# Kernel optimization log

Measured on AMD Instinct MI355X. Metric: run time of the kernel, lower is better.

The kernel has to match this reference:

```python
import jax, jax.numpy as jnp
import numpy as np

N = 50000; E = 800000; B = 5000
ND = 32; ED = 16; HD = 64; H = 128; L = 3
IN_DIM = ND + 2 * H  # 288, GNN in_channels
NEG = 0.2  # GATv2 leaky_relu slope
EPS = 1e-5  # LayerNorm eps


def silu(x):
    return x * jax.nn.sigmoid(x)


def layer_norm(x, g, b):
    mu = jnp.mean(x, -1, keepdims=True)
    v = jnp.var(x, -1, keepdims=True)
    return (x - mu) * jax.lax.rsqrt(v + EPS) * g + b


def setup_inputs() -> dict:
    key = jax.random.key(0)
    ks = iter(jax.random.split(key, 48))

    def w(shape):
        return jax.random.normal(next(ks), shape, jnp.float32) * 0.02

    inp = {}
    inp['x_t'] = jax.random.normal(next(ks), (N, ND), jnp.float32)
    inp['t'] = jax.random.randint(next(ks), (N,), 0, 1000)
    inp['household_features'] = jax.random.normal(next(ks), (B, HD), jnp.float32)
    inp['edge_index'] = jax.random.randint(next(ks), (2, E), 0, N)
    inp['edge_attr'] = jax.random.normal(next(ks), (E, ED), jnp.float32)
    inp['batch'] = jnp.sort(jax.random.randint(next(ks), (N,), 0, B))
    z = jnp.zeros; o = jnp.ones
    inp.update(dict(
        tW1=w((1, H)), tb1=z(H), tW2=w((H, H)), tb2=z(H),
        hW1=w((HD, H)), hb1=z(H), hg1=o(H), hB1=z(H),
        hW2=w((H, H)), hb2=z(H), hg2=o(H), hB2=z(H),
        Wl=w((L, IN_DIM, H)), bl=z((L, H)), Wr=w((L, IN_DIM, H)), br=z((L, H)),
        We=w((L, ED, H)), att=w((L, H)), gb=z((L, H)),
        fcpW=w((H, IN_DIM)), fcpb=z(IN_DIM),
        npW1=w((H, H)), npb1=z(H), npg=o(H), npB=z(H),
        npW2=w((H, ND)), npb2=z(ND)))
    return inp


def reference(x_t, t, household_features, edge_index, edge_attr, batch,
              tW1, tb1, tW2, tb2,
              hW1, hb1, hg1, hB1, hW2, hb2, hg2, hB2,
              Wl, bl, Wr, br, We, att, gb,
              fcpW, fcpb, npW1, npb1, npg, npB, npW2, npb2):
    # time embedding: Linear(1,H) -> SiLU -> Linear(H,H)
    t_emb = silu(t[:, None].astype(jnp.float32) @ tW1 + tb1) @ tW2 + tb2
    # household encoder: (Linear, LN, SiLU) x2, then gather per node
    h = silu(layer_norm(household_features @ hW1 + hb1, hg1, hB1))
    h = silu(layer_norm(h @ hW2 + hb2, hg2, hB2))
    x = jnp.concatenate([x_t, t_emb, h[batch]], axis=1)  # [N, IN_DIM]

    # add self loops (PyG default), edge_attr filled with per-feature mean
    loop = jnp.arange(N)
    src = jnp.concatenate([edge_index[0], loop])
    dst = jnp.concatenate([edge_index[1], loop])
    ea = jnp.concatenate([edge_attr, jnp.broadcast_to(edge_attr.mean(0), (N, ED))], axis=0)

    for l in range(L):  # GATv2Conv layers (heads=1)
        xl = x @ Wl[l] + bl[l]  # [N, H] source transform
        xr = x @ Wr[l] + br[l]  # [N, H] target transform
        m = jax.nn.leaky_relu(xl[src] + xr[dst] + ea @ We[l], NEG)  # [Etot, H]
        score = m @ att[l]  # [Etot]
        smax = jax.ops.segment_max(score, dst, num_segments=N)
        ex = jnp.exp(score - smax[dst])
        denom = jax.ops.segment_sum(ex, dst, num_segments=N) + 1e-16
        alpha = ex / denom[dst]
        out = jax.ops.segment_sum(alpha[:, None] * xl[src], dst, num_segments=N) + gb[l]
        x = silu(out)
        if l < L - 1:
            x = x @ fcpW + fcpb  # fc_projection back to IN_DIM
    # node_projection: Linear, LN, SiLU, Linear
    return silu(layer_norm(x @ npW1 + npb1, npg, npB)) @ npW2 + npb2
```

## Files before the change

### kernel.cpp

```cpp
#include <hip/hip_runtime.h>
#include <hip/hip_bf16.h>

#define NN 50000
#define NE 800000
#define NB 5000
#define ND 32
#define EDD 16
#define HDD 64
#define H 128
#define ETOT (NE + NN)
#define NEG 0.2f
#define EPS_LN 1e-5f

typedef float pf2 __attribute__((ext_vector_type(2)));

__device__ __forceinline__ float siluf(float x){ return x / (1.f + __expf(-x)); }

__device__ __forceinline__ float wsum(float v){
  v += __shfl_xor(v, 32, 64);
  v += __shfl_xor(v, 16, 64);
  v += __shfl_xor(v, 8, 64);
  v += __shfl_xor(v, 4, 64);
  v += __shfl_xor(v, 2, 64);
  v += __shfl_xor(v, 1, 64);
  return v;
}

#define DPP_ADD(v, ctrl) \
  v += __builtin_bit_cast(float, __builtin_amdgcn_update_dpp(0, __builtin_bit_cast(int, v), ctrl, 0xf, 0xf, true))
__device__ __forceinline__ float wsum_bcast(float v){
  DPP_ADD(v, 0x111);
  DPP_ADD(v, 0x112);
  DPP_ADD(v, 0x114);
  DPP_ADD(v, 0x118);
  DPP_ADD(v, 0x142);
  DPP_ADD(v, 0x143);
  return __builtin_bit_cast(float, __builtin_amdgcn_readlane(__builtin_bit_cast(int, v), 63));
}

__device__ __forceinline__ float blockLN128(float x, const float* g, const float* b, int j, float* red){
  int lane = j & 63, wid = j >> 6;
  float s = wsum(x);
  if (lane == 0) red[wid] = s;
  __syncthreads();
  float mu = (red[0] + red[1]) * 0.0078125f;
  float d = x - mu;
  float s2 = wsum(d * d);
  if (lane == 0) red[2 + wid] = s2;
  __syncthreads();
  float var = (red[2] + red[3]) * 0.0078125f;
  return d * (1.f / sqrtf(var + EPS_LN)) * g[j] + b[j];
}

__global__ __launch_bounds__(128) void k_house(const float* __restrict__ hf,
    const float* __restrict__ hW1, const float* __restrict__ hb1,
    const float* __restrict__ hg1, const float* __restrict__ hB1,
    const float* __restrict__ hW2, const float* __restrict__ hb2,
    const float* __restrict__ hg2, const float* __restrict__ hB2,
    float* __restrict__ hout){
  __shared__ float sin_[HDD];
  __shared__ float smid[H];
  __shared__ float red[4];
  int bidx = blockIdx.x, j = threadIdx.x;
  if (j < HDD) sin_[j] = hf[bidx * HDD + j];
  __syncthreads();
  float acc = hb1[j];
  #pragma unroll
  for (int k = 0; k < HDD; k++) acc += sin_[k] * hW1[k * H + j];
  float v = siluf(blockLN128(acc, hg1, hB1, j, red));
  __syncthreads();
  smid[j] = v;
  __syncthreads();
  float acc2 = hb2[j];
  #pragma unroll
  for (int k = 0; k < H; k++) acc2 += smid[k] * hW2[k * H + j];
  float v2 = siluf(blockLN128(acc2, hg2, hB2, j, red));
  hout[bidx * H + j] = v2;
}

__global__ __launch_bounds__(128) void k_temb(const float* __restrict__ tW1, const float* __restrict__ tb1,
    const float* __restrict__ tW2, const float* __restrict__ tb2, float* __restrict__ table){
  __shared__ float smid[H];
  int bidx = blockIdx.x, j = threadIdx.x;
  float tv = (float)bidx;
  smid[j] = siluf(tv * tW1[j] + tb1[j]);
  __syncthreads();
  float acc = tb2[j];
  #pragma unroll
  for (int k = 0; k < H; k++) acc += smid[k] * tW2[k * H + j];
  table[bidx * H + j] = acc;
}

__global__ __launch_bounds__(256) void k_gemm(const float* __restrict__ A, const float* __restrict__ W,
    const float* __restrict__ bias, float* __restrict__ C, int M, int K, int Nc){
  __shared__ float As[16][68];
  __shared__ float Ws[16][64];
  int t = threadIdx.x;
  int m0 = blockIdx.x * 64, n0 = blockIdx.y * 64;
  int tx = t & 15, ty = t >> 4;
  int la_m = t >> 2, la_k = (t & 3) << 2;
  int lw_k = t >> 4, lw_j = (t & 15) << 2;
  float acc[4][4] = {{0.f}};
  int arow = m0 + la_m;
  for (int k0 = 0; k0 < K; k0 += 16){
    float4 a = make_float4(0.f, 0.f, 0.f, 0.f);
    if (arow < M) a = *(const float4*)(A + (size_t)arow * K + k0 + la_k);
    As[la_k + 0][la_m] = a.x; As[la_k + 1][la_m] = a.y;
    As[la_k + 2][la_m] = a.z; As[la_k + 3][la_m] = a.w;
    float4 wv = make_float4(0.f, 0.f, 0.f, 0.f);
    if (n0 + lw_j < Nc) wv = *(const float4*)(W + (size_t)(k0 + lw_k) * Nc + n0 + lw_j);
    *(float4*)&Ws[lw_k][lw_j] = wv;
    __syncthreads();
    #pragma unroll
    for (int k = 0; k < 16; k++){
      float4 a4 = *(const float4*)&As[k][ty << 2];
      float4 b4 = *(const float4*)&Ws[k][tx << 2];
      acc[0][0] += a4.x * b4.x; acc[0][1] += a4.x * b4.y; acc[0][2] += a4.x * b4.z; acc[0][3] += a4.x * b4.w;
      acc[1][0] += a4.y * b4.x; acc[1][1] += a4.y * b4.y; acc[1][2] += a4.y * b4.z; acc[1][3] += a4.y * b4.w;
      acc[2][0] += a4.z * b4.x; acc[2][1] += a4.z * b4.y; acc[2][2] += a4.z * b4.z; acc[2][3] += a4.z * b4.w;
      acc[3][0] += a4.w * b4.x; acc[3][1] += a4.w * b4.y; acc[3][2] += a4.w * b4.z; acc[3][3] += a4.w * b4.w;
    }
    __syncthreads();
  }
  int col = n0 + (tx << 2);
  if (col < Nc){
    float4 b4 = make_float4(0.f, 0.f, 0.f, 0.f);
    if (bias) b4 = *(const float4*)(bias + col);
    #pragma unroll
    for (int r = 0; r < 4; r++){
      int row = m0 + (ty << 2) + r;
      if (row < M){
        float4 o = make_float4(acc[r][0] + b4.x, acc[r][1] + b4.y, acc[r][2] + b4.z, acc[r][3] + b4.w);
        *(float4*)(C + (size_t)row * Nc + col) = o;
      }
    }
  }
}

__global__ __launch_bounds__(256) void k_gemm128(const float* __restrict__ A, const float* __restrict__ W,
    const float* __restrict__ bias, float* __restrict__ C, int M, int K, int Nc){
  __shared__ float As[16][132];
  __shared__ float Ws[16][128];
  int t = threadIdx.x;
  int m0 = blockIdx.x * 128, n0 = blockIdx.y * 128;
  int tx = t & 15, ty = t >> 4;
  float acc[8][8];
  #pragma unroll
  for (int r = 0; r < 8; r++)
    #pragma unroll
    for (int c = 0; c < 8; c++) acc[r][c] = 0.f;
  for (int k0 = 0; k0 < K; k0 += 16){
    #pragma unroll
    for (int l = 0; l < 2; l++){
      int idx = t + l * 256;
      int ar = idx >> 2, ac = (idx & 3) << 2;
      float4 a = make_float4(0.f, 0.f, 0.f, 0.f);
      if (m0 + ar < M) a = *(const float4*)(A + (size_t)(m0 + ar) * K + k0 + ac);
      As[ac + 0][ar] = a.x; As[ac + 1][ar] = a.y;
      As[ac + 2][ar] = a.z; As[ac + 3][ar] = a.w;
    }
    #pragma unroll
    for (int l = 0; l < 2; l++){
      int idx = t + l * 256;
      int wr = idx >> 5, wc = (idx & 31) << 2;
      float4 wv = make_float4(0.f, 0.f, 0.f, 0.f);
      if (n0 + wc < Nc) wv = *(const float4*)(W + (size_t)(k0 + wr) * Nc + n0 + wc);
      *(float4*)&Ws[wr][wc] = wv;
    }
    __syncthreads();
    #pragma unroll
    for (int k = 0; k < 16; k++){
      float4 a0 = *(const float4*)&As[k][ty * 8];
      float4 a1 = *(const float4*)&As[k][ty * 8 + 4];
      float4 b0 = *(const float4*)&Ws[k][tx * 8];
      float4 b1 = *(const float4*)&Ws[k][tx * 8 + 4];
      float ar_[8] = {a0.x, a0.y, a0.z, a0.w, a1.x, a1.y, a1.z, a1.w};
      float bc_[8] = {b0.x, b0.y, b0.z, b0.w, b1.x, b1.y, b1.z, b1.w};
      #pragma unroll
      for (int r = 0; r < 8; r++)
        #pragma unroll
        for (int c = 0; c < 8; c++) acc[r][c] += ar_[r] * bc_[c];
    }
    __syncthreads();
  }
  int col = n0 + tx * 8;
  float4 bb0 = make_float4(0.f, 0.f, 0.f, 0.f), bb1 = bb0;
  if (bias && col < Nc){ bb0 = *(const float4*)(bias + col); bb1 = *(const float4*)(bias + col + 4); }
  #pragma unroll
  for (int r = 0; r < 8; r++){
    int row = m0 + ty * 8 + r;
    if (row < M && col < Nc){
      float4 o0 = make_float4(acc[r][0] + bb0.x, acc[r][1] + bb0.y, acc[r][2] + bb0.z, acc[r][3] + bb0.w);
      float4 o1 = make_float4(acc[r][4] + bb1.x, acc[r][5] + bb1.y, acc[r][6] + bb1.z, acc[r][7] + bb1.w);
      *(float4*)(C + (size_t)row * Nc + col) = o0;
      *(float4*)(C + (size_t)row * Nc + col + 4) = o1;
    }
  }
}

__global__ __launch_bounds__(256) void k_gemmln(const float* __restrict__ A, const float* __restrict__ W,
    const float* __restrict__ bias, const float* __restrict__ g, const float* __restrict__ B,
    float* __restrict__ out, int M){
  __shared__ float As[16][132];
  __shared__ float Ws[16][128];
  int t = threadIdx.x;
  int m0 = blockIdx.x * 128;
  int tx = t & 15, ty = t >> 4;
  float acc[8][8];
  #pragma unroll
  for (int r = 0; r < 8; r++)
    #pragma unroll
    for (int c = 0; c < 8; c++) acc[r][c] = 0.f;
  for (int k0 = 0; k0 < H; k0 += 16){
    #pragma unroll
    for (int l = 0; l < 2; l++){
      int idx = t + l * 256;
      int ar = idx >> 2, ac = (idx & 3) << 2;
      float4 a = make_float4(0.f, 0.f, 0.f, 0.f);
      if (m0 + ar < M) a = *(const float4*)(A + (size_t)(m0 + ar) * H + k0 + ac);
      As[ac + 0][ar] = a.x; As[ac + 1][ar] = a.y;
      As[ac + 2][ar] = a.z; As[ac + 3][ar] = a.w;
    }
    #pragma unroll
    for (int l = 0; l < 2; l++){
      int idx = t + l * 256;
      int wr = idx >> 5, wc = (idx & 31) << 2;
      *(float4*)&Ws[wr][wc] = *(const float4*)(W + (size_t)(k0 + wr) * H + wc);
    }
    __syncthreads();
    #pragma unroll
    for (int k = 0; k < 16; k++){
      float4 a0 = *(const float4*)&As[k][ty * 8];
      float4 a1 = *(const float4*)&As[k][ty * 8 + 4];
      float4 b0 = *(const float4*)&Ws[k][tx * 8];
      float4 b1 = *(const float4*)&Ws[k][tx * 8 + 4];
      float ar_[8] = {a0.x, a0.y, a0.z, a0.w, a1.x, a1.y, a1.z, a1.w};
      float bc_[8] = {b0.x, b0.y, b0.z, b0.w, b1.x, b1.y, b1.z, b1.w};
      #pragma unroll
      for (int r = 0; r < 8; r++)
        #pragma unroll
        for (int c = 0; c < 8; c++) acc[r][c] += ar_[r] * bc_[c];
    }
    __syncthreads();
  }
  int col = tx * 8;
  float bb[8], gv[8], Bv[8];
  *(float4*)&bb[0] = *(const float4*)(bias + col); *(float4*)&bb[4] = *(const float4*)(bias + col + 4);
  *(float4*)&gv[0] = *(const float4*)(g + col);    *(float4*)&gv[4] = *(const float4*)(g + col + 4);
  *(float4*)&Bv[0] = *(const float4*)(B + col);    *(float4*)&Bv[4] = *(const float4*)(B + col + 4);
  #pragma unroll
  for (int r = 0; r < 8; r++){
    int row = m0 + ty * 8 + r;
    if (row >= M) continue;
    float v[8];
    float s = 0.f;
    #pragma unroll
    for (int c = 0; c < 8; c++){ v[c] = acc[r][c] + bb[c]; s += v[c]; }
    s += __shfl_xor(s, 1, 16); s += __shfl_xor(s, 2, 16);
    s += __shfl_xor(s, 4, 16); s += __shfl_xor(s, 8, 16);
    float mu = s * 0.0078125f;
    float s2 = 0.f;
    #pragma unroll
    for (int c = 0; c < 8; c++){ v[c] -= mu; s2 += v[c] * v[c]; }
    s2 += __shfl_xor(s2, 1, 16); s2 += __shfl_xor(s2, 2, 16);
    s2 += __shfl_xor(s2, 4, 16); s2 += __shfl_xor(s2, 8, 16);
    float rstd = 1.f / sqrtf(s2 * 0.0078125f + EPS_LN);
    float o[8];
    #pragma unroll
    for (int c = 0; c < 8; c++) o[c] = siluf(v[c] * rstd * gv[c] + Bv[c]);
    *(float4*)(out + (size_t)row * H + col) = *(float4*)&o[0];
    *(float4*)(out + (size_t)row * H + col + 4) = *(float4*)&o[4];
  }
}

__global__ void k_packs(const float* __restrict__ Wl, const float* __restrict__ Wr,
    float* __restrict__ W0h, float* __restrict__ W0m, float* __restrict__ W0t,
    float* __restrict__ Wp1, float* __restrict__ Wp2){
  int r = blockIdx.x, L = blockIdx.y, c = threadIdx.x;
  float v = (c < H) ? Wl[(size_t)L * 288 * H + r * H + c] : Wr[(size_t)L * 288 * H + r * H + (c - H)];
  if (L == 0){
    if (r < 32) W0h[r * 256 + c] = v;
    else if (r < 160) W0m[(r - 32) * 256 + c] = v;
    else W0t[(r - 160) * 256 + c] = v;
  } else {
    (L == 1 ? Wp1 : Wp2)[r * 256 + c] = v;
  }
}
__global__ void k_small(const float* __restrict__ bl, const float* __restrict__ br,
    const float* __restrict__ Wl, const float* __restrict__ Wr, const float* __restrict__ fcpb,
    float* __restrict__ b0, float* __restrict__ cc1, float* __restrict__ cc2, float* __restrict__ eam){
  int c = threadIdx.x, which = blockIdx.x;
  if (which == 0){
    b0[c] = (c < H) ? bl[c] : br[c - H];
    if (c < 16) eam[c] *= (1.f / NE);
  } else {
    int cc = (c < H) ? c : c - H;
    const float* Wsrc = ((c < H) ? Wl : Wr) + (size_t)which * 288 * H;
    float acc = (c < H) ? bl[which * H + cc] : br[which * H + cc];
    for (int k = 0; k < 288; k++) acc += fcpb[k] * Wsrc[k * H + cc];
    (which == 1 ? cc1 : cc2)[c] = acc;
  }
}

__global__ __launch_bounds__(256) void k_xlr0(const float* __restrict__ x_t, const int* __restrict__ tt,
    const int* __restrict__ batch, const float* __restrict__ T0, const float* __restrict__ H0,
    const float* __restrict__ Whead, const float* __restrict__ b0, float* __restrict__ xlr){
  __shared__ float sx[4][ND];
  __shared__ int sti[4], sbi[4];
  int b4 = blockIdx.x * 4;
  int t = threadIdx.x;
  if (t < 128){
    int n = t >> 5, k = t & 31;
    int i = b4 + n;
    if (i < NN) sx[n][k] = x_t[(size_t)i * ND + k];
  }
  if (t < 4){
    int i = b4 + t;
    if (i < NN){ sti[t] = tt[i]; sbi[t] = batch[i]; }
  }
  __syncthreads();
  int wid = t >> 6, lane = t & 63;
  int i = b4 + wid;
  if (i >= NN) return;
  int c = lane << 2;
  float4 acc = *(const float4*)(b0 + c);
  float4 tv = *(const float4*)(T0 + (size_t)sti[wid] * 256 + c);
  float4 hv = *(const float4*)(H0 + (size_t)sbi[wid] * 256 + c);
  acc.x += tv.x + hv.x; acc.y += tv.y + hv.y; acc.z += tv.z + hv.z; acc.w += tv.w + hv.w;
  #pragma unroll
  for (int k = 0; k < ND; k++){
    float xk = sx[wid][k];
    float4 wv = *(const float4*)(Whead + k * 256 + c);
    acc.x += xk * wv.x; acc.y += xk * wv.y; acc.z += xk * wv.z; acc.w += xk * wv.w;
  }
  *(float4*)(xlr + (size_t)i * 256 + c) = acc;
}

__global__ void k_edge_mean(const float* __restrict__ ea, float* __restrict__ sum16){
  __shared__ float ss[16];
  int t = threadIdx.x;
  if (t < 16) ss[t] = 0.f;
  __syncthreads();
  float p[16];
  #pragma unroll
  for (int k = 0; k < 16; k++) p[k] = 0.f;
  for (int r = blockIdx.x * blockDim.x + t; r < NE; r += gridDim.x * blockDim.x){
    const float4* rp = (const float4*)(ea + (size_t)r * 16);
    float4 q0 = rp[0], q1 = rp[1], q2 = rp[2], q3 = rp[3];
    p[0] += q0.x; p[1] += q0.y; p[2] += q0.z; p[3] += q0.w;
    p[4] += q1.x; p[5] += q1.y; p[6] += q1.z; p[7] += q1.w;
    p[8] += q2.x; p[9] += q2.y; p[10] += q2.z; p[11] += q2.w;
    p[12] += q3.x; p[13] += q3.y; p[14] += q3.z; p[15] += q3.w;
  }
  #pragma unroll
  for (int k = 0; k < 16; k++) atomicAdd(&ss[k], p[k]);
  __syncthreads();
  if (t < 16) atomicAdd(&sum16[t], ss[t]);
}

__global__ void k_deg_count(const int* __restrict__ eidx, int* __restrict__ deg){
  int e = blockIdx.x * 256 + threadIdx.x;
  if (e < NE) atomicAdd(&deg[eidx[NE + e]], 1);
}
__global__ __launch_bounds__(256) void k_scan1(const int* __restrict__ deg, int* __restrict__ row_ptr, int* __restrict__ bs){
  __shared__ int sc[256];
  int t = threadIdx.x;
  int base = blockIdx.x * 1024 + t * 4;
  int v0 = (base + 0 < NN) ? deg[base + 0] + 1 : 0;
  int v1 = (base + 1 < NN) ? deg[base + 1] + 1 : 0;
  int v2 = (base + 2 < NN) ? deg[base + 2] + 1 : 0;
  int v3 = (base + 3 < NN) ? deg[base + 3] + 1 : 0;
  int s0 = v0, s1 = s0 + v1, s2 = s1 + v2, s3 = s2 + v3;
  sc[t] = s3;
  __syncthreads();
  for (int off = 1; off < 256; off <<= 1){
    int add = (t >= off) ? sc[t - off] : 0;
    __syncthreads();
    sc[t] += add;
    __syncthreads();
  }
  int excl = sc[t] - s3;
  if (base + 0 < NN) row_ptr[base + 1] = excl + s0;
  if (base + 1 < NN) row_ptr[base + 2] = excl + s1;
  if (base + 2 < NN) row_ptr[base + 3] = excl + s2;
  if (base + 3 < NN) row_ptr[base + 4] = excl + s3;
  if (t == 255) bs[blockIdx.x] = sc[255];
}
__global__ void k_scan2(int* __restrict__ bs, int nb){
  int lane = threadIdx.x;
  int v = (lane < nb) ? bs[lane] : 0;
  for (int off = 1; off < 64; off <<= 1){
    int n = __shfl_up(v, off, 64);
    if (lane >= off) v += n;
  }
  if (lane < nb) bs[lane] = v;
}
__global__ void k_scan3(int* __restrict__ row_ptr, const int* __restrict__ bs,
    const int* __restrict__ deg, int* __restrict__ fill){
  int i = blockIdx.x * 256 + threadIdx.x;
  if (i == 0) row_ptr[0] = 0;
  if (i < NN){
    int chunk = i >> 10;
    int rp1 = row_ptr[i + 1] + ((chunk > 0) ? bs[chunk - 1] : 0);
    row_ptr[i + 1] = rp1;
    fill[i] = rp1 - deg[i] - 1;
  }
}
__global__ void k_fill_edges(const int* __restrict__ eidx, int* __restrict__ fill,
    int* __restrict__ csrc, int* __restrict__ ceid){
  int e = blockIdx.x * 256 + threadIdx.x;
  if (e < NE){
    int d = eidx[NE + e];
    int pos = atomicAdd(&fill[d], 1);
    csrc[pos] = eidx[e];
    ceid[pos] = e;
  }
}
__global__ void k_fill_self(int* __restrict__ fill, int* __restrict__ csrc, int* __restrict__ ceid){
  int i = blockIdx.x * 256 + threadIdx.x;
  if (i < NN){
    int pos = atomicAdd(&fill[i], 1);
    csrc[pos] = i;
    ceid[pos] = NE;
  }
}

__global__ __launch_bounds__(256) void k_sagg(const float* __restrict__ xlr,
    const float* __restrict__ ea, const float* __restrict__ eamean,
    const float* __restrict__ Wel, const float* __restrict__ attl, const float* __restrict__ gbl,
    const int* __restrict__ row_ptr, const int* __restrict__ csrc, const int* __restrict__ ceid,
    float* __restrict__ y){
  int t = threadIdx.x;
  int wid = t >> 6, lane = t & 63;
  int i = blockIdx.x * 4 + wid;
  if (i >= NN) return;
  int dim = lane << 1;
  pf2 rW[16];
  #pragma unroll
  for (int k = 0; k < 16; k++) rW[k] = *(const pf2*)(Wel + k * H + dim);
  pf2 xr2 = *(const pf2*)(xlr + (size_t)i * 256 + H + dim);
  pf2 a2 = *(const pf2*)(attl + dim);
  int row = __builtin_amdgcn_readfirstlane(row_ptr[i]);
  int end = __builtin_amdgcn_readfirstlane(row_ptr[i + 1]);
  float m = -1e30f, den = 0.f;
  pf2 acc2; acc2.x = 0.f; acc2.y = 0.f;
  for (int p = row; p < end; ++p){
    int s   = __builtin_amdgcn_readfirstlane(csrc[p]);
    int eid = __builtin_amdgcn_readfirstlane(ceid[p]);
    pf2 vl = *(const pf2*)(xlr + (size_t)s * 256 + dim);
    const float* ep = (eid < NE) ? (ea + (size_t)eid * 16) : eamean;
    pf2 ew; ew.x = 0.f; ew.y = 0.f;
    #pragma unroll
    for (int k = 0; k < 16; k++) ew += rW[k] * ep[k];
    pf2 vv = vl + xr2 + ew;
    pf2 vn = vv * NEG;
    vv.x = fmaxf(vv.x, vn.x);
    vv.y = fmaxf(vv.y, vn.y);
    pf2 sp = a2 * vv;
    float sc = wsum_bcast(sp.x + sp.y);
    if (sc <= m){
      float wv = __expf(sc - m);
      den += wv;
      acc2 += vl * wv;
    } else {
      float scale = __expf(m - sc);
      den = den * scale + 1.f;
      acc2 = acc2 * scale + vl;
      m = sc;
    }
  }
  float inv = 1.f / (den + 1e-16f);
  pf2 gb2 = *(const pf2*)(gbl + dim);
  pf2 o = acc2 * inv + gb2;
  o.x = siluf(o.x); o.y = siluf(o.y);
  *(pf2*)(y + (size_t)i * H + dim) = o;
}

extern "C" void kernel_launch(void* const* d_in, const int* in_sizes, int n_in,
                              void* d_out, int out_size, void* d_ws, size_t ws_size,
                              hipStream_t stream){
  (void)in_sizes; (void)n_in; (void)out_size; (void)ws_size;
  const float* x_t  = (const float*)d_in[0];
  const int*   t    = (const int*)d_in[1];
  const float* hf   = (const float*)d_in[2];
  const int*   eidx = (const int*)d_in[3];
  const float* ea   = (const float*)d_in[4];
  const int*   batch= (const int*)d_in[5];
  const float* tW1  = (const float*)d_in[6];
  const float* tb1  = (const float*)d_in[7];
  const float* tW2  = (const float*)d_in[8];
  const float* tb2  = (const float*)d_in[9];
  const float* hW1  = (const float*)d_in[10];
  const float* hb1  = (const float*)d_in[11];
  const float* hg1  = (const float*)d_in[12];
  const float* hB1  = (const float*)d_in[13];
  const float* hW2  = (const float*)d_in[14];
  const float* hb2  = (const float*)d_in[15];
  const float* hg2  = (const float*)d_in[16];
  const float* hB2  = (const float*)d_in[17];
  const float* Wl   = (const float*)d_in[18];
  const float* bl   = (const float*)d_in[19];
  const float* Wr   = (const float*)d_in[20];
  const float* br   = (const float*)d_in[21];
  const float* We   = (const float*)d_in[22];
  const float* att  = (const float*)d_in[23];
  const float* gb   = (const float*)d_in[24];
  const float* fcpW = (const float*)d_in[25];
  const float* fcpb = (const float*)d_in[26];
  const float* npW1 = (const float*)d_in[27];
  const float* npb1 = (const float*)d_in[28];
  const float* npg  = (const float*)d_in[29];
  const float* npB  = (const float*)d_in[30];
  const float* npW2 = (const float*)d_in[31];
  const float* npb2 = (const float*)d_in[32];

  char* w = (char*)d_ws;
  size_t off = 0;
  auto alloc = [&](size_t bytes) -> void* {
    void* p = w + off;
    off += (bytes + 255) & ~(size_t)255;
    return p;
  };
  float* table = (float*)alloc((size_t)1000 * H * 4);
  float* hbuf  = (float*)alloc((size_t)NB * H * 4);
  float* T0    = (float*)alloc((size_t)1000 * 256 * 4);
  float* H0b   = (float*)alloc((size_t)NB * 256 * 4);
  float* W0h   = (float*)alloc((size_t)32 * 256 * 4);
  float* W0m   = (float*)alloc((size_t)128 * 256 * 4);
  float* W0t   = (float*)alloc((size_t)128 * 256 * 4);
  float* b0    = (float*)alloc(256 * 4);
  float* Wp1   = (float*)alloc((size_t)288 * 256 * 4);
  float* Wp2   = (float*)alloc((size_t)288 * 256 * 4);
  float* Ac1   = (float*)alloc((size_t)128 * 256 * 4);
  float* Ac2   = (float*)alloc((size_t)128 * 256 * 4);
  float* cc1   = (float*)alloc(256 * 4);
  float* cc2   = (float*)alloc(256 * 4);
  float* eam   = (float*)alloc(16 * 4);
  int* deg     = (int*)alloc((size_t)NN * 4);
  int* row_ptr = (int*)alloc((size_t)(NN + 1) * 4);
  int* fill    = (int*)alloc((size_t)NN * 4);
  int* bs      = (int*)alloc(64 * 4);
  int* csrc    = (int*)alloc((size_t)ETOT * 4);
  int* ceid    = (int*)alloc((size_t)ETOT * 4);
  float* xlr   = (float*)alloc((size_t)NN * 256 * 4);
  float* y     = (float*)alloc((size_t)NN * H * 4);
  float* z2 = xlr;

  hipMemsetAsync(eam, 0, 64, stream);
  hipMemsetAsync(deg, 0, (size_t)NN * 4, stream);
  k_edge_mean<<<512, 256, 0, stream>>>(ea, eam);
  k_small<<<3, 256, 0, stream>>>(bl, br, Wl, Wr, fcpb, b0, cc1, cc2, eam);
  k_house<<<NB, 128, 0, stream>>>(hf, hW1, hb1, hg1, hB1, hW2, hb2, hg2, hB2, hbuf);
  k_temb<<<1000, 128, 0, stream>>>(tW1, tb1, tW2, tb2, table);
  k_deg_count<<<(NE + 255) / 256, 256, 0, stream>>>(eidx, deg);
  k_scan1<<<49, 256, 0, stream>>>(deg, row_ptr, bs);
  k_scan2<<<1, 64, 0, stream>>>(bs, 49);
  k_scan3<<<(NN + 255) / 256, 256, 0, stream>>>(row_ptr, bs, deg, fill);
  k_fill_edges<<<(NE + 255) / 256, 256, 0, stream>>>(eidx, fill, csrc, ceid);
  k_fill_self<<<(NN + 255) / 256, 256, 0, stream>>>(fill, csrc, ceid);
  k_packs<<<dim3(288, 3), 256, 0, stream>>>(Wl, Wr, W0h, W0m, W0t, Wp1, Wp2);
  auto gemm = [&](const float* A, const float* W_, const float* bias, float* C, int M, int K, int Nc){
    dim3 g((M + 63) / 64, (Nc + 63) / 64);
    k_gemm<<<g, 256, 0, stream>>>(A, W_, bias, C, M, K, Nc);
  };
  auto gemm128 = [&](const float* A, const float* W_, const float* bias, float* C, int M, int K, int Nc){
    dim3 g((M + 127) / 128, (Nc + 127) / 128);
    k_gemm128<<<g, 256, 0, stream>>>(A, W_, bias, C, M, K, Nc);
  };
  gemm128(table, W0m, nullptr, T0, 1000, H, 256);
  gemm128(hbuf, W0t, nullptr, H0b, NB, H, 256);
  gemm(fcpW, Wp1, nullptr, Ac1, H, 288, 256);
  gemm(fcpW, Wp2, nullptr, Ac2, H, 288, 256);
  k_xlr0<<<(NN + 3) / 4, 256, 0, stream>>>(x_t, t, batch, T0, H0b, W0h, b0, xlr);
  k_sagg<<<(NN + 3) / 4, 256, 0, stream>>>(xlr, ea, eam, We, att, gb, row_ptr, csrc, ceid, y);
  gemm128(y, Ac1, cc1, xlr, NN, H, 256);
  k_sagg<<<(NN + 3) / 4, 256, 0, stream>>>(xlr, ea, eam, We + 16 * H, att + H, gb + H, row_ptr, csrc, ceid, y);
  gemm128(y, Ac2, cc2, xlr, NN, H, 256);
  k_sagg<<<(NN + 3) / 4, 256, 0, stream>>>(xlr, ea, eam, We + 32 * H, att + 2 * H, gb + 2 * H, row_ptr, csrc, ceid, y);
  k_gemmln<<<(NN + 127) / 128, 256, 0, stream>>>(y, npW1, npb1, npg, npB, z2, NN);
  gemm(z2, npW2, npb2, (float*)d_out, NN, H, ND);
}
```

Before: 959.1 us.

## Split edge softmax into two streams, pack CSR arrays, reuse gemmln for household

The per-node edge aggregation loop now runs two independent online-softmax accumulators over alternating edges and merges them at the end. The goal is to shorten the serial dependency chain and overlap gathers. The CSR source and edge-id arrays are packed into one int2 array, so each edge needs one load instead of two. The household encoder drops its per-row block kernel and makes two calls to the tiled GEMM+LayerNorm kernel, which now takes K as a parameter. Both changes add some register pressure and an extra intermediate buffer.

```diff
diff --git a/kernel.cpp b/kernel.cpp
--- a/kernel.cpp
+++ b/kernel.cpp
@@ -36,46 +36,6 @@
   DPP_ADD(v, 0x142);
   DPP_ADD(v, 0x143);
   return __builtin_bit_cast(float, __builtin_amdgcn_readlane(__builtin_bit_cast(int, v), 63));
-}
-
-__device__ __forceinline__ float blockLN128(float x, const float* g, const float* b, int j, float* red){
-  int lane = j & 63, wid = j >> 6;
-  float s = wsum(x);
-  if (lane == 0) red[wid] = s;
-  __syncthreads();
-  float mu = (red[0] + red[1]) * 0.0078125f;
-  float d = x - mu;
-  float s2 = wsum(d * d);
-  if (lane == 0) red[2 + wid] = s2;
-  __syncthreads();
-  float var = (red[2] + red[3]) * 0.0078125f;
-  return d * (1.f / sqrtf(var + EPS_LN)) * g[j] + b[j];
-}
-
-__global__ __launch_bounds__(128) void k_house(const float* __restrict__ hf,
-    const float* __restrict__ hW1, const float* __restrict__ hb1,
-    const float* __restrict__ hg1, const float* __restrict__ hB1,
-    const float* __restrict__ hW2, const float* __restrict__ hb2,
-    const float* __restrict__ hg2, const float* __restrict__ hB2,
-    float* __restrict__ hout){
-  __shared__ float sin_[HDD];
-  __shared__ float smid[H];
-  __shared__ float red[4];
-  int bidx = blockIdx.x, j = threadIdx.x;
-  if (j < HDD) sin_[j] = hf[bidx * HDD + j];
-  __syncthreads();
-  float acc = hb1[j];
-  #pragma unroll
-  for (int k = 0; k < HDD; k++) acc += sin_[k] * hW1[k * H + j];
-  float v = siluf(blockLN128(acc, hg1, hB1, j, red));
-  __syncthreads();
-  smid[j] = v;
-  __syncthreads();
-  float acc2 = hb2[j];
-  #pragma unroll
-  for (int k = 0; k < H; k++) acc2 += smid[k] * hW2[k * H + j];
-  float v2 = siluf(blockLN128(acc2, hg2, hB2, j, red));
-  hout[bidx * H + j] = v2;
 }
 
 __global__ __launch_bounds__(128) void k_temb(const float* __restrict__ tW1, const float* __restrict__ tb1,
@@ -200,7 +160,7 @@
 
 __global__ __launch_bounds__(256) void k_gemmln(const float* __restrict__ A, const float* __restrict__ W,
     const float* __restrict__ bias, const float* __restrict__ g, const float* __restrict__ B,
-    float* __restrict__ out, int M){
+    float* __restrict__ out, int M, int K){
   __shared__ float As[16][132];
   __shared__ float Ws[16][128];
   int t = threadIdx.x;
@@ -211,13 +171,13 @@
   for (int r = 0; r < 8; r++)
     #pragma unroll
     for (int c = 0; c < 8; c++) acc[r][c] = 0.f;
-  for (int k0 = 0; k0 < H; k0 += 16){
+  for (int k0 = 0; k0 < K; k0 += 16){
     #pragma unroll
     for (int l = 0; l < 2; l++){
       int idx = t + l * 256;
       int ar = idx >> 2, ac = (idx & 3) << 2;
       float4 a = make_float4(0.f, 0.f, 0.f, 0.f);
-      if (m0 + ar < M) a = *(const float4*)(A + (size_t)(m0 + ar) * H + k0 + ac);
+      if (m0 + ar < M) a = *(const float4*)(A + (size_t)(m0 + ar) * K + k0 + ac);
       As[ac + 0][ar] = a.x; As[ac + 1][ar] = a.y;
       As[ac + 2][ar] = a.z; As[ac + 3][ar] = a.w;
     }
@@ -407,28 +367,26 @@
   }
 }
 __global__ void k_fill_edges(const int* __restrict__ eidx, int* __restrict__ fill,
-    int* __restrict__ csrc, int* __restrict__ ceid){
+    int2* __restrict__ cse){
   int e = blockIdx.x * 256 + threadIdx.x;
   if (e < NE){
     int d = eidx[NE + e];
     int pos = atomicAdd(&fill[d], 1);
-    csrc[pos] = eidx[e];
-    ceid[pos] = e;
-  }
-}
-__global__ void k_fill_self(int* __restrict__ fill, int* __restrict__ csrc, int* __restrict__ ceid){
+    cse[pos] = make_int2(eidx[e], e);
+  }
+}
+__global__ void k_fill_self(int* __restrict__ fill, int2* __restrict__ cse){
   int i = blockIdx.x * 256 + threadIdx.x;
   if (i < NN){
     int pos = atomicAdd(&fill[i], 1);
-    csrc[pos] = i;
-    ceid[pos] = NE;
+    cse[pos] = make_int2(i, NE);
   }
 }
 
 __global__ __launch_bounds__(256) void k_sagg(const float* __restrict__ xlr,
     const float* __restrict__ ea, const float* __restrict__ eamean,
     const float* __restrict__ Wel, const float* __restrict__ attl, const float* __restrict__ gbl,
-    const int* __restrict__ row_ptr, const int* __restrict__ csrc, const int* __restrict__ ceid,
+    const int* __restrict__ row_ptr, const int2* __restrict__ cse,
     float* __restrict__ y){
   int t = threadIdx.x;
   int wid = t >> 6, lane = t & 63;
@@ -442,11 +400,14 @@
   pf2 a2 = *(const pf2*)(attl + dim);
   int row = __builtin_amdgcn_readfirstlane(row_ptr[i]);
   int end = __builtin_amdgcn_readfirstlane(row_ptr[i + 1]);
-  float m = -1e30f, den = 0.f;
+  float m1 = -1e30f, den1 = 0.f;
+  float m2 = -1e30f, den2 = 0.f;
+  pf2 acc1; acc1.x = 0.f; acc1.y = 0.f;
   pf2 acc2; acc2.x = 0.f; acc2.y = 0.f;
-  for (int p = row; p < end; ++p){
-    int s   = __builtin_amdgcn_readfirstlane(csrc[p]);
-    int eid = __builtin_amdgcn_readfirstlane(ceid[p]);
+  auto edge = [&](int p, float& m, float& den, pf2& acc){
+    int2 se = cse[p];
+    int s   = __builtin_amdgcn_readfirstlane(se.x);
+    int eid = __builtin_amdgcn_readfirstlane(se.y);
     pf2 vl = *(const pf2*)(xlr + (size_t)s * 256 + dim);
     const float* ep = (eid < NE) ? (ea + (size_t)eid * 16) : eamean;
     pf2 ew; ew.x = 0.f; ew.y = 0.f;
@@ -461,17 +422,27 @@
     if (sc <= m){
       float wv = __expf(sc - m);
       den += wv;
-      acc2 += vl * wv;
+      acc += vl * wv;
     } else {
-      float scale = __expf(m - sc);
-      den = den * scale + 1.f;
-      acc2 = acc2 * scale + vl;
+      float f = __expf(m - sc);
+      den = den * f + 1.f;
+      acc = acc * f + vl;
       m = sc;
     }
-  }
+  };
+  int p = row;
+  for (; p + 1 < end; p += 2){
+    edge(p, m1, den1, acc1);
+    edge(p + 1, m2, den2, acc2);
+  }
+  if (p < end) edge(p, m1, den1, acc1);
+  float M = fmaxf(m1, m2);
+  float f1 = __expf(m1 - M), f2 = __expf(m2 - M);
+  float den = den1 * f1 + den2 * f2;
+  pf2 acc = acc1 * f1 + acc2 * f2;
   float inv = 1.f / (den + 1e-16f);
   pf2 gb2 = *(const pf2*)(gbl + dim);
-  pf2 o = acc2 * inv + gb2;
+  pf2 o = acc * inv + gb2;
   o.x = siluf(o.x); o.y = siluf(o.y);
   *(pf2*)(y + (size_t)i * H + dim) = o;
 }
@@ -522,6 +493,7 @@
     return p;
   };
   float* table = (float*)alloc((size_t)1000 * H * 4);
+  float* hbuf1 = (float*)alloc((size_t)NB * H * 4);
   float* hbuf  = (float*)alloc((size_t)NB * H * 4);
   float* T0    = (float*)alloc((size_t)1000 * 256 * 4);
   float* H0b   = (float*)alloc((size_t)NB * 256 * 4);
@@ -540,8 +512,7 @@
   int* row_ptr = (int*)alloc((size_t)(NN + 1) * 4);
   int* fill    = (int*)alloc((size_t)NN * 4);
   int* bs      = (int*)alloc(64 * 4);
-  int* csrc    = (int*)alloc((size_t)ETOT * 4);
-  int* ceid    = (int*)alloc((size_t)ETOT * 4);
+  int2* cse    = (int2*)alloc((size_t)ETOT * 8);
   float* xlr   = (float*)alloc((size_t)NN * 256 * 4);
   float* y     = (float*)alloc((size_t)NN * H * 4);
   float* z2 = xlr;
@@ -550,14 +521,15 @@
   hipMemsetAsync(deg, 0, (size_t)NN * 4, stream);
   k_edge_mean<<<512, 256, 0, stream>>>(ea, eam);
   k_small<<<3, 256, 0, stream>>>(bl, br, Wl, Wr, fcpb, b0, cc1, cc2, eam);
-  k_house<<<NB, 128, 0, stream>>>(hf, hW1, hb1, hg1, hB1, hW2, hb2, hg2, hB2, hbuf);
+  k_gemmln<<<(NB + 127) / 128, 256, 0, stream>>>(hf, hW1, hb1, hg1, hB1, hbuf1, NB, HDD);
+  k_gemmln<<<(NB + 127) / 128, 256, 0, stream>>>(hbuf1, hW2, hb2, hg2, hB2, hbuf, NB, H);
   k_temb<<<1000, 128, 0, stream>>>(tW1, tb1, tW2, tb2, table);
   k_deg_count<<<(NE + 255) / 256, 256, 0, stream>>>(eidx, deg);
   k_scan1<<<49, 256, 0, stream>>>(deg, row_ptr, bs);
   k_scan2<<<1, 64, 0, stream>>>(bs, 49);
   k_scan3<<<(NN + 255) / 256, 256, 0, stream>>>(row_ptr, bs, deg, fill);
-  k_fill_edges<<<(NE + 255) / 256, 256, 0, stream>>>(eidx, fill, csrc, ceid);
-  k_fill_self<<<(NN + 255) / 256, 256, 0, stream>>>(fill, csrc, ceid);
+  k_fill_edges<<<(NE + 255) / 256, 256, 0, stream>>>(eidx, fill, cse);
+  k_fill_self<<<(NN + 255) / 256, 256, 0, stream>>>(fill, cse);
   k_packs<<<dim3(288, 3), 256, 0, stream>>>(Wl, Wr, W0h, W0m, W0t, Wp1, Wp2);
   auto gemm = [&](const float* A, const float* W_, const float* bias, float* C, int M, int K, int Nc){
     dim3 g((M + 63) / 64, (Nc + 63) / 64);
@@ -572,11 +544,11 @@
   gemm(fcpW, Wp1, nullptr, Ac1, H, 288, 256);
   gemm(fcpW, Wp2, nullptr, Ac2, H, 288, 256);
   k_xlr0<<<(NN + 3) / 4, 256, 0, stream>>>(x_t, t, batch, T0, H0b, W0h, b0, xlr);
-  k_sagg<<<(NN + 3) / 4, 256, 0, stream>>>(xlr, ea, eam, We, att, gb, row_ptr, csrc, ceid, y);
+  k_sagg<<<(NN + 3) / 4, 256, 0, stream>>>(xlr, ea, eam, We, att, gb, row_ptr, cse, y);
   gemm128(y, Ac1, cc1, xlr, NN, H, 256);
-  k_sagg<<<(NN + 3) / 4, 256, 0, stream>>>(xlr, ea, eam, We + 16 * H, att + H, gb + H, row_ptr, csrc, ceid, y);
+  k_sagg<<<(NN + 3) / 4, 256, 0, stream>>>(xlr, ea, eam, We + 16 * H, att + H, gb + H, row_ptr, cse, y);
   gemm128(y, Ac2, cc2, xlr, NN, H, 256);
-  k_sagg<<<(NN + 3) / 4, 256, 0, stream>>>(xlr, ea, eam, We + 32 * H, att + 2 * H, gb + 2 * H, row_ptr, csrc, ceid, y);
-  k_gemmln<<<(NN + 127) / 128, 256, 0, stream>>>(y, npW1, npb1, npg, npB, z2, NN);
+  k_sagg<<<(NN + 3) / 4, 256, 0, stream>>>(xlr, ea, eam, We + 32 * H, att + 2 * H, gb + 2 * H, row_ptr, cse, y);
+  k_gemmln<<<(NN + 127) / 128, 256, 0, stream>>>(y, npW1, npb1, npg, npB, z2, NN, H);
   gemm(z2, npW2, npb2, (float*)d_out, NN, H, ND);
 }
```

Measured after the change: 950.1 us. About the same (-0.9%).
